# Performance work log

Hardware: AMD Instinct MI355X
Metric: run time of the kernel (lower is better)

Reference implementation:

```python
import jax, jax.numpy as jnp
import numpy as np
from jax import lax

EPS = 1e-5
MIN_SAMPLES = 4
RESHAPE = 14        # edge-map downsample factor
KEEP_FRAC = 0.1     # 1 - quantile(0.9)
KERNEL_FRAC = 0.05  # eval-mode log_kernel

SOBEL_X = jnp.array([[-1., 0., 1.], [-2., 0., 2.], [-1., 0., 1.]], jnp.float32)
SOBEL_Y = jnp.array([[-1., -2., -1.], [0., 0., 0.], [1., 2., 1.]], jnp.float32)


def _dwconv3(x, k):
    C = x.shape[1]
    kern = jnp.broadcast_to(k, (C, 1, 3, 3)).astype(x.dtype)
    return lax.conv_general_dilated(x, kern, (1, 1), 'SAME',
        feature_group_count=C, dimension_numbers=('NCHW', 'OIHW', 'NCHW'))


def _erode3(m):
    k = jnp.ones((1, 1, 3, 3), m.dtype)
    s = lax.conv_general_dilated(m, k, (1, 1), 'SAME',
        dimension_numbers=('NCHW', 'OIHW', 'NCHW'))
    return (s >= 9.0).astype(m.dtype)


def _masked_mean(x, mask, axis=-1):
    m = mask.astype(x.dtype)
    return jnp.sum(x * m, axis=axis) / jnp.maximum(jnp.sum(m, axis=axis), 1.0)


def _ssi_norm(x, mask):
    # scale-shift-invariant normalization: masked median shift, masked MAD scale
    big = jnp.where(mask, x, jnp.inf)
    srt = jnp.sort(big, axis=-1)
    n = jnp.sum(mask, axis=-1)
    idx = jnp.maximum((n - 1) // 2, 0)
    med = jnp.take_along_axis(srt, idx[..., None], axis=-1)
    med = jnp.where(n[..., None] > 0, med, 0.0)
    scale = _masked_mean(jnp.abs(x - med), mask, axis=-1)[..., None]
    return (x - med) / jnp.maximum(scale, EPS)


def _get_edge(image, vmask):
    gx = _dwconv3(image, SOBEL_X) / 8.0
    gy = _dwconv3(image, SOBEL_Y) / 8.0
    gx = jnp.sqrt(jnp.mean(gx * gx, axis=1, keepdims=True))
    gy = jnp.sqrt(jnp.mean(gy * gy, axis=1, keepdims=True))
    edges = jnp.sqrt(gx * gx + gy * gy)
    H, W = edges.shape[-2:]
    bm = jnp.zeros((H, W), edges.dtype).at[3:H - 3, 3:W - 3].set(1.0)
    return edges * bm * vmask


def _resize_bilinear(x, oh, ow):
    # torch F.interpolate bilinear, align_corners=False, no antialias
    B, C, H, W = x.shape
    def coords(o, s):
        c = jnp.clip((jnp.arange(o) + 0.5) * (s / o) - 0.5, 0.0, s - 1.0)
        i0 = jnp.floor(c).astype(jnp.int32)
        return i0, jnp.minimum(i0 + 1, s - 1), c - i0
    y0, y1, wy = coords(oh, H)
    x0, x1, wx = coords(ow, W)
    wy = wy[:, None]; wx = wx[None, :]
    g = lambda yi, xi: x[:, :, yi[:, None], xi[None, :]]
    return (g(y0, x0) * (1 - wy) * (1 - wx) + g(y0, x1) * (1 - wy) * wx
          + g(y1, x0) * wy * (1 - wx) + g(y1, x1) * wy * wx)


def _sample_edges(edges):
    B, _, H, W = edges.shape
    oh, ow = H // RESHAPE, W // RESHAPE
    e = _resize_bilinear(edges, oh, ow).reshape(B, -1)
    k = max(int(KEEP_FRAC * oh * ow), 10)
    _, idx = lax.top_k(e, k)
    return jnp.stack([(idx // ow) * RESHAPE, (idx % ow) * RESHAPE], -1).astype(jnp.int32)


def _extract_patches(x, coords, kh, kw):
    # vectorized irregular patch gather: [B,C,H,W] + [B,P,2] -> [B,P*C,kh*kw]
    B, C, H, W = x.shape
    ph, pw = kh // 2, kw // 2
    xp = jnp.pad(x, ((0, 0), (0, 0), (ph, ph), (pw, pw)))
    dy = jnp.arange(-ph, ph + 1)
    dx = jnp.arange(-pw, pw + 1)
    def one(img, y, x_):
        return img[:, (y + dy)[:, None], (x_ + dx)[None, :]]
    patches = jax.vmap(jax.vmap(one, in_axes=(None, 0, 0)))(
        xp, coords[..., 0] + ph, coords[..., 1] + pw)  # [B,P,C,kh,kw]
    return patches.reshape(B, -1, kh * kw)


def _forward(inp, tgt, mask, image, vmask):
    mask = mask.astype(bool)
    inp = inp.astype(jnp.float32)
    tgt = tgt.astype(jnp.float32)
    B, _, H, W = inp.shape
    vm = _erode3(vmask.astype(jnp.float32))
    edges = _get_edge(image.astype(jnp.float32), vm)
    coords = _sample_edges(edges)
    ks = int(KERNEL_FRAC * min(H, W))
    ks += int(ks % 2 == 0)
    # local patch branch
    pin = _extract_patches(inp, coords, ks, ks)
    ptg = _extract_patches(tgt, coords, ks, ks)
    pmk = _extract_patches(mask.astype(jnp.float32), coords, ks, ks) > 0.5
    pin = _ssi_norm(pin, pmk)
    ptg = _ssi_norm(ptg, pmk)
    err = jnp.maximum(jnp.abs(pin - ptg), EPS)
    valid = jnp.sum(pmk, axis=-1) >= MIN_SAMPLES
    ep = jnp.sqrt(jnp.maximum(_masked_mean(err, pmk, -1), EPS))  # [B,P]
    e_patch = _masked_mean(ep, valid, -1)                         # [B]
    # global image branch
    gi = _ssi_norm(inp.reshape(B, 1, H * W), mask.reshape(B, 1, H * W))
    gt = _ssi_norm(tgt.reshape(B, 1, H * W), mask.reshape(B, 1, H * W))
    gerr = jnp.maximum(jnp.abs(gi - gt), EPS)
    e_glob = jnp.sqrt(jnp.maximum(_masked_mean(gerr, mask.reshape(B, 1, H * W), -1), EPS)).squeeze(-1)
    return 0.5 * (e_patch + e_glob)  # [B]


def setup_inputs() -> dict:
    key = jax.random.key(0)
    k1, k2, k3, k4 = jax.random.split(key, 4)
    B, H, W = 32, 480, 640
    return {
        'input': jax.random.uniform(k1, (B, 1, H, W), jnp.float32, 0.1, 10.0),
        'target': jax.random.uniform(k2, (B, 1, H, W), jnp.float32, 0.1, 10.0),
        'mask': jax.random.bernoulli(k3, 0.9, (B, 1, H, W)),
        'image': jax.random.normal(k4, (B, 3, H, W), jnp.float32),
        'validity_mask': jnp.ones((B, 1, H, W), bool),
    }


def reference(input, target, mask, image, validity_mask):
    return _forward(input, target, mask, image, validity_mask)
```

## Files before the change

kernel.cpp:

```cpp
#include <hip/hip_runtime.h>
#include <math.h>

#define BB 32
#define HH 480
#define WW 640
#define HWN (HH * WW)
#define OH 34
#define OW 45
#define OHW (OH * OW)
#define KTOP 153
#define KS 25
#define PHW 12
#define PATCH (KS * KS)
#define RESHAPE_I 14
#define EPSV 1e-5f

#define TSLICE 10
#define TSW (OHW / TSLICE)

#define NB12 4096
#define PSLICE 32
#define NSLICE 16
#define CAP 32768
#define LCAP 2048
#define CPAD 32

#define EDGE_BLKS ((BB * OHW * 4) / 256)
#define RANK_BLKS (BB * TSLICE)
#define COL_BLKS (BB * 2 * NSLICE)

__device__ __forceinline__ unsigned int fkey(float f) {
  unsigned int u = __float_as_uint(f);
  return (u & 0x80000000u) ? ~u : (u | 0x80000000u);
}
__device__ __forceinline__ float fkey_inv(unsigned int k) {
  unsigned int u = (k & 0x80000000u) ? (k & 0x7FFFFFFFu) : ~k;
  return __uint_as_float(u);
}

__device__ __forceinline__ float breduce256(float v, float* red) {
  const int t = threadIdx.x;
  __syncthreads();
  red[t] = v;
  __syncthreads();
  for (int s2 = 128; s2 > 0; s2 >>= 1) {
    if (t < s2) red[t] += red[t + s2];
    __syncthreads();
  }
  float r = red[0];
  __syncthreads();
  return r;
}

__device__ __forceinline__ float2 breduce256x2(float a, float b, float* red) {
  const int t = threadIdx.x;
  __syncthreads();
  red[t] = a;
  red[256 + t] = b;
  __syncthreads();
  for (int s2 = 128; s2 > 0; s2 >>= 1) {
    if (t < s2) {
      red[t] += red[t + s2];
      red[256 + t] += red[256 + t + s2];
    }
    __syncthreads();
  }
  float2 r = make_float2(red[0], red[256]);
  __syncthreads();
  return r;
}

__device__ float edge_at(const float* __restrict__ image, const unsigned char* __restrict__ vmask,
                         int b, int y, int x) {
  if (y < 3 || y >= HH - 3 || x < 3 || x >= WW - 3) return 0.f;
  const unsigned char* vm = vmask + (size_t)b * HWN;
  #pragma unroll
  for (int dy = -1; dy <= 1; ++dy) {
    #pragma unroll
    for (int dx = -1; dx <= 1; ++dx) {
      if (!vm[(size_t)(y + dy) * WW + (x + dx)]) return 0.f;
    }
  }
  const float* img = image + (size_t)b * 3 * HWN;
  float sx2 = 0.f, sy2 = 0.f;
  #pragma unroll
  for (int c = 0; c < 3; ++c) {
    const float* p = img + (size_t)c * HWN + (size_t)y * WW + x;
    float a00 = p[-WW - 1], a01 = p[-WW], a02 = p[-WW + 1];
    float a10 = p[-1],                    a12 = p[1];
    float a20 = p[WW - 1],  a21 = p[WW],  a22 = p[WW + 1];
    float gx = (-a00 + a02 + -2.f * a10 + 2.f * a12 + -a20 + a22) / 8.f;
    float gy = (-a00 + -2.f * a01 + -a02 + a20 + 2.f * a21 + a22) / 8.f;
    sx2 += gx * gx;
    sy2 += gy * gy;
  }
  float gxm = sqrtf(sx2 / 3.f);
  float gym = sqrtf(sy2 / 3.f);
  return sqrtf(gxm * gxm + gym * gym);
}

__global__ __launch_bounds__(256) void gpass12_kernel(const float* __restrict__ inp,
                                                      const float* __restrict__ tgt,
                                                      const unsigned char* __restrict__ mask,
                                                      unsigned int* __restrict__ ghist) {
  const int b = blockIdx.x / PSLICE;
  const int sl = blockIdx.x % PSLICE;
  const int t = threadIdx.x;
  __shared__ unsigned int hist[2 * NB12];
  for (int i = t; i < 2 * NB12; i += 256) hist[i] = 0;
  __syncthreads();
  const float4* xi4 = (const float4*)(inp + (size_t)b * HWN);
  const float4* xt4 = (const float4*)(tgt + (size_t)b * HWN);
  const unsigned int* m4 = (const unsigned int*)(mask + (size_t)b * HWN);
  const int per4 = (HWN / PSLICE) / 4;
  const int s0 = sl * per4;
  for (int i = s0 + t; i < s0 + per4; i += 256) {
    unsigned int mm = m4[i];
    if (!mm) continue;
    float4 a = xi4[i], c = xt4[i];
    if (mm & 0x000000FFu) { atomicAdd(&hist[fkey(a.x) >> 20], 1u); atomicAdd(&hist[NB12 + (fkey(c.x) >> 20)], 1u); }
    if (mm & 0x0000FF00u) { atomicAdd(&hist[fkey(a.y) >> 20], 1u); atomicAdd(&hist[NB12 + (fkey(c.y) >> 20)], 1u); }
    if (mm & 0x00FF0000u) { atomicAdd(&hist[fkey(a.z) >> 20], 1u); atomicAdd(&hist[NB12 + (fkey(c.z) >> 20)], 1u); }
    if (mm & 0xFF000000u) { atomicAdd(&hist[fkey(a.w) >> 20], 1u); atomicAdd(&hist[NB12 + (fkey(c.w) >> 20)], 1u); }
  }
  __syncthreads();
  for (int i = t; i < NB12; i += 256) {
    unsigned int h0 = hist[i], h1 = hist[NB12 + i];
    if (h0) atomicAdd(&ghist[(size_t)(b * 2 + 0) * NB12 + i], h0);
    if (h1) atomicAdd(&ghist[(size_t)(b * 2 + 1) * NB12 + i], h1);
  }
}

__global__ __launch_bounds__(256) void edge_resize_kernel(const float* __restrict__ image,
                                                          const unsigned char* __restrict__ vmask,
                                                          float* __restrict__ re) {
  int gid = blockIdx.x * 256 + threadIdx.x;
  int corner = gid & 3;
  int cell = gid >> 2;
  int b = cell / OHW;
  int rem = cell % OHW;
  int oy = rem / OW, ox = rem % OW;

  const float ry = (float)((double)HH / (double)OH);
  const float rx = (float)((double)WW / (double)OW);
  float cy = fminf(fmaxf(((float)oy + 0.5f) * ry - 0.5f, 0.f), (float)(HH - 1));
  float cx = fminf(fmaxf(((float)ox + 0.5f) * rx - 0.5f, 0.f), (float)(WW - 1));
  int y0 = (int)floorf(cy);
  int x0 = (int)floorf(cx);
  int y1 = min(y0 + 1, HH - 1);
  int x1 = min(x0 + 1, WW - 1);
  float wy = cy - (float)y0;
  float wx = cx - (float)x0;

  int yy = (corner & 2) ? y1 : y0;
  int xx = (corner & 1) ? x1 : x0;
  float w = ((corner & 2) ? wy : 1.f - wy) * ((corner & 1) ? wx : 1.f - wx);
  float g = edge_at(image, vmask, b, yy, xx) * w;
  g += __shfl_xor(g, 1, 64);
  g += __shfl_xor(g, 2, 64);
  if (corner == 0) re[cell] = g;
}

__global__ __launch_bounds__(256) void k_rank_sel(const float* __restrict__ re,
                                                  const unsigned int* __restrict__ ghist,
                                                  int* __restrict__ rpart,
                                                  int* __restrict__ sel) {
  __shared__ float e[OHW];
  __shared__ unsigned int scan[256];
  const int t = threadIdx.x;
  if (blockIdx.x < RANK_BLKS) {
    const int b = blockIdx.x / TSLICE;
    const int sl = blockIdx.x % TSLICE;
    for (int i = t; i < OHW; i += 256) e[i] = re[b * OHW + i];
    __syncthreads();

    float vi[6];
    int idx[6], cnt[6];
    #pragma unroll
    for (int q = 0; q < 6; ++q) {
      int i = t + q * 256;
      idx[q] = i;
      vi[q] = (i < OHW) ? e[i] : 0.f;
      cnt[q] = 0;
    }
    const int j0 = sl * TSW;
    for (int jj = 0; jj < TSW; ++jj) {
      int j = j0 + jj;
      float u = e[j];
      #pragma unroll
      for (int q = 0; q < 6; ++q) {
        cnt[q] += (u > vi[q]) || (u == vi[q] && j < idx[q]);
      }
    }
    int* rp = rpart + ((size_t)b * TSLICE + sl) * OHW;
    #pragma unroll
    for (int q = 0; q < 6; ++q) {
      if (idx[q] < OHW) rp[idx[q]] = cnt[q];
    }
  } else {
    const int bs = blockIdx.x - RANK_BLKS;
    const unsigned int* gh = ghist + (size_t)bs * NB12;
    unsigned int local[16];
    unsigned int s = 0;
    const int base = t * 16;
    #pragma unroll
    for (int j = 0; j < 16; ++j) {
      local[j] = gh[base + j];
      s += local[j];
    }
    scan[t] = s;
    __syncthreads();
    for (int d = 1; d < 256; d <<= 1) {
      unsigned int v = (t >= d) ? scan[t - d] : 0u;
      __syncthreads();
      scan[t] += v;
      __syncthreads();
    }
    const unsigned int incl = scan[t];
    const unsigned int ex = incl - s;
    const unsigned int n = scan[255];
    if (n == 0) {
      if (t == 0) {
        sel[bs * 4 + 0] = -1;
        sel[bs * 4 + 1] = 0;
        sel[bs * 4 + 2] = 0;
        sel[bs * 4 + 3] = 0;
      }
      return;
    }
    const unsigned int r = (n - 1) >> 1;
    if (r >= ex && r < incl) {
      unsigned int cum = ex;
      int bin = base;
      #pragma unroll
      for (int j = 0; j < 16; ++j) {
        unsigned int h = local[j];
        if (cum + h > r) { bin = base + j; break; }
        cum += h;
      }
      sel[bs * 4 + 0] = bin;
      sel[bs * 4 + 1] = (int)(r - cum);
      sel[bs * 4 + 2] = (int)n;
      sel[bs * 4 + 3] = (int)cum;
    }
  }
}

__global__ __launch_bounds__(256) void k_write_collect(const float* __restrict__ inp,
                                                       const float* __restrict__ tgt,
                                                       const unsigned char* __restrict__ mask,
                                                       const int* __restrict__ sel,
                                                       const int* __restrict__ rpart,
                                                       float* __restrict__ cand,
                                                       unsigned int* __restrict__ ccount,
                                                       float* __restrict__ sbelow,
                                                       float* __restrict__ sabove,
                                                       int* __restrict__ coords) {
  __shared__ float red[512];
  __shared__ float buf[LCAP];
  __shared__ unsigned int lcnt, gbase;
  const int t = threadIdx.x;
  if (blockIdx.x < COL_BLKS) {
    const int bs = blockIdx.x / NSLICE;
    const int sl = blockIdx.x % NSLICE;
    const int b = bs >> 1, s = bs & 1;
    const float* x = (s == 0 ? inp : tgt) + (size_t)b * HWN;
    const unsigned char* m = mask + (size_t)b * HWN;
    const int prefix = sel[bs * 4 + 0];
    if (t == 0) lcnt = 0;
    __syncthreads();
    float sb = 0.f, sa = 0.f;
    if (prefix >= 0) {
      float* cd = cand + (size_t)bs * CAP;
      const float4* x4 = (const float4*)x;
      const unsigned int* m4 = (const unsigned int*)m;
      const int per4 = (HWN / NSLICE) / 4;
      const int s0 = sl * per4;
      for (int i = s0 + t; i < s0 + per4; i += 256) {
        unsigned int mm = m4[i];
        if (!mm) continue;
        float4 a = x4[i];
        #define GCOL(av, bit) \
          if (mm & bit) { \
            float v = av; \
            int pf = (int)(fkey(v) >> 20); \
            if (pf < prefix) sb += v; \
            else if (pf > prefix) sa += v; \
            else { \
              unsigned int pos = atomicAdd(&lcnt, 1u); \
              if (pos < LCAP) buf[pos] = v; \
              else { \
                unsigned int g = atomicAdd(&ccount[bs * CPAD], 1u); \
                if (g < CAP) cd[g] = v; \
              } \
            } \
          }
        GCOL(a.x, 0x000000FFu)
        GCOL(a.y, 0x0000FF00u)
        GCOL(a.z, 0x00FF0000u)
        GCOL(a.w, 0xFF000000u)
        #undef GCOL
      }
    }
    __syncthreads();
    if (prefix >= 0) {
      unsigned int c = min(lcnt, (unsigned int)LCAP);
      if (t == 0 && c > 0) gbase = atomicAdd(&ccount[bs * CPAD], c);
      __syncthreads();
      if (c > 0) {
        float* cd = cand + (size_t)bs * CAP;
        unsigned int base = gbase;
        for (unsigned int i = t; i < c; i += 256) {
          unsigned int pos = base + i;
          if (pos < CAP) cd[pos] = buf[i];
        }
      }
    }
    float2 ts = breduce256x2(sb, sa, red);
    if (t == 0) {
      atomicAdd(&sbelow[bs], ts.x);
      atomicAdd(&sabove[bs], ts.y);
    }
  } else {
    const int b = blockIdx.x - COL_BLKS;
    const int* rp = rpart + (size_t)b * TSLICE * OHW;
    for (int i = t; i < OHW; i += 256) {
      int rank = 0;
      #pragma unroll
      for (int sl = 0; sl < TSLICE; ++sl) rank += rp[sl * OHW + i];
      if (rank < KTOP) {
        coords[(b * KTOP + rank) * 2 + 0] = (i / OW) * RESHAPE_I;
        coords[(b * KTOP + rank) * 2 + 1] = (i % OW) * RESHAPE_I;
      }
    }
  }
}

__global__ __launch_bounds__(64, 4) void patch_kernel(const float* __restrict__ inp,
                                                      const float* __restrict__ tgt,
                                                      const unsigned char* __restrict__ mask,
                                                      const int* __restrict__ coords,
                                                      float* __restrict__ ep, float* __restrict__ val) {
  const int bk = blockIdx.x;
  const int b = bk / KTOP;
  const int t = threadIdx.x;
  __shared__ unsigned int hist[512];
  __shared__ unsigned int sh_pref[2];
  __shared__ int sh_rank[2];

  const int cy = coords[bk * 2 + 0];
  const int cx = coords[bk * 2 + 1];

  float v_in[10], v_tg[10];
  unsigned int mbits = 0;
  #pragma unroll
  for (int q = 0; q < 10; ++q) {
    int i = t + q * 64;
    float vi = 0.f, vt = 0.f;
    if (i < PATCH) {
      int dy = i / KS - PHW, dx = i % KS - PHW;
      int y = cy + dy, x = cx + dx;
      if (y >= 0 && y < HH && x >= 0 && x < WW) {
        size_t off = (size_t)b * HWN + (size_t)y * WW + x;
        if (mask[off]) mbits |= (1u << q);
        vi = inp[off];
        vt = tgt[off];
      }
    }
    v_in[q] = vi; v_tg[q] = vt;
  }

  int pn = __popc(mbits);
  #pragma unroll
  for (int d = 32; d > 0; d >>= 1) pn += __shfl_xor(pn, d, 64);
  const int n = pn;
  const float nf = (float)n;
  const int r = (n > 0) ? ((n - 1) >> 1) : 0;

  if (t == 0) {
    sh_pref[0] = 0; sh_pref[1] = 0;
    sh_rank[0] = r; sh_rank[1] = r;
  }
  __syncthreads();

  #pragma unroll
  for (int p = 0; p < 4; ++p) {
    const int shift = 24 - 8 * p;
    #pragma unroll
    for (int j = 0; j < 8; ++j) hist[t + 64 * j] = 0;
    __syncthreads();
    const int r_in = sh_rank[0], r_tg = sh_rank[1];
    const unsigned int pref_in = sh_pref[0], pref_tg = sh_pref[1];
    #pragma unroll
    for (int q = 0; q < 10; ++q) {
      if (mbits & (1u << q)) {
        unsigned int k = fkey(v_in[q]);
        if (p == 0 || (k >> (shift + 8)) == pref_in)
          atomicAdd(&hist[(k >> shift) & 255u], 1u);
        unsigned int k2 = fkey(v_tg[q]);
        if (p == 0 || (k2 >> (shift + 8)) == pref_tg)
          atomicAdd(&hist[256 + ((k2 >> shift) & 255u)], 1u);
      }
    }
    __syncthreads();
    {
      unsigned int a0 = hist[t * 4 + 0], a1 = hist[t * 4 + 1];
      unsigned int a2 = hist[t * 4 + 2], a3 = hist[t * 4 + 3];
      unsigned int b0 = hist[256 + t * 4 + 0], b1 = hist[256 + t * 4 + 1];
      unsigned int b2 = hist[256 + t * 4 + 2], b3 = hist[256 + t * 4 + 3];
      unsigned int sa0 = a0, sa1 = sa0 + a1, sa2 = sa1 + a2, sa3 = sa2 + a3;
      unsigned int sb0 = b0, sb1 = sb0 + b1, sb2 = sb1 + b2, sb3 = sb2 + b3;
      unsigned int ta = sa3, tb = sb3;
      #pragma unroll
      for (int d = 1; d < 64; d <<= 1) {
        unsigned int ua = (unsigned int)__shfl_up((int)ta, d, 64);
        unsigned int ub = (unsigned int)__shfl_up((int)tb, d, 64);
        if (t >= d) { ta += ua; tb += ub; }
      }
      unsigned int exa = ta - sa3, exb = tb - sb3;
      unsigned int rra = (unsigned int)r_in, rrb = (unsigned int)r_tg;
      unsigned int pa[4] = {exa, exa + sa0, exa + sa1, exa + sa2};
      unsigned int ca[4] = {exa + sa0, exa + sa1, exa + sa2, exa + sa3};
      unsigned int pb[4] = {exb, exb + sb0, exb + sb1, exb + sb2};
      unsigned int cb[4] = {exb + sb0, exb + sb1, exb + sb2, exb + sb3};
      #pragma unroll
      for (int j = 0; j < 4; ++j) {
        if (rra >= pa[j] && rra < ca[j]) {
          sh_pref[0] = (pref_in << 8) | (unsigned int)(t * 4 + j);
          sh_rank[0] = (int)(rra - pa[j]);
        }
        if (rrb >= pb[j] && rrb < cb[j]) {
          sh_pref[1] = (pref_tg << 8) | (unsigned int)(t * 4 + j);
          sh_rank[1] = (int)(rrb - pb[j]);
        }
      }
    }
    __syncthreads();
  }

  const float med_i = (n > 0) ? fkey_inv(sh_pref[0]) : 0.f;
  const float med_t = (n > 0) ? fkey_inv(sh_pref[1]) : 0.f;

  float pi = 0.f, pt = 0.f;
  #pragma unroll
  for (int q = 0; q < 10; ++q) {
    if (mbits & (1u << q)) {
      pi += fabsf(v_in[q] - med_i);
      pt += fabsf(v_tg[q] - med_t);
    }
  }
  #pragma unroll
  for (int d = 32; d > 0; d >>= 1) {
    pi += __shfl_xor(pi, d, 64);
    pt += __shfl_xor(pt, d, 64);
  }
  const float si = fmaxf(pi / fmaxf(nf, 1.f), EPSV);
  const float st = fmaxf(pt / fmaxf(nf, 1.f), EPSV);

  float pe = 0.f;
  #pragma unroll
  for (int q = 0; q < 10; ++q) {
    if (mbits & (1u << q)) {
      float a = (v_in[q] - med_i) / si;
      float c = (v_tg[q] - med_t) / st;
      pe += fmaxf(fabsf(a - c), EPSV);
    }
  }
  #pragma unroll
  for (int d = 32; d > 0; d >>= 1) pe += __shfl_xor(pe, d, 64);

  if (t == 0) {
    ep[bk] = sqrtf(fmaxf(pe / fmaxf(nf, 1.f), EPSV));
    val[bk] = (n >= 4) ? 1.f : 0.f;
  }
}

__global__ __launch_bounds__(256) void k_gfinal_preduce(const float* __restrict__ cand,
                                                        const unsigned int* __restrict__ ccount,
                                                        const int* __restrict__ sel,
                                                        const float* __restrict__ sbelow,
                                                        const float* __restrict__ sabove,
                                                        const float* __restrict__ ep,
                                                        const float* __restrict__ val,
                                                        float* __restrict__ gstats,
                                                        float* __restrict__ nvals,
                                                        float* __restrict__ e_patch) {
  __shared__ unsigned int hist[256];
  __shared__ float red[512];
  __shared__ int sh_bin, sh_r;
  __shared__ float sh_med;
  const int t = threadIdx.x;
  if (blockIdx.x < 64) {
    const int bs = blockIdx.x;
    const int prefix = sel[bs * 4 + 0];
    const int r2 = sel[bs * 4 + 1];
    const int n = sel[bs * 4 + 2];
    const int nbelow = sel[bs * 4 + 3];
    const float* cd = cand + (size_t)bs * CAP;
    int c = (int)min(ccount[bs * CPAD], (unsigned int)CAP);
    if (prefix < 0) {
      if (t == 0) {
        gstats[bs * 2 + 0] = 0.f;
        gstats[bs * 2 + 1] = 0.f;
        if ((bs & 1) == 0) nvals[bs >> 1] = 0.f;
      }
      return;
    }

    hist[t] = 0;
    __syncthreads();
    for (int i = t; i < c; i += 256)
      atomicAdd(&hist[(fkey(cd[i]) >> 12) & 255u], 1u);
    __syncthreads();
    if (t == 0) {
      unsigned int rr = (unsigned int)r2, cum = 0;
      int bin = 0;
      for (; bin < 256; ++bin) {
        unsigned int h = hist[bin];
        if (cum + h > rr) break;
        cum += h;
      }
      sh_bin = bin;
      sh_r = (int)(rr - cum);
    }
    __syncthreads();
    const int bin1 = sh_bin;
    const int r3 = sh_r;

    hist[t] = 0;
    __syncthreads();
    for (int i = t; i < c; i += 256) {
      unsigned int k = fkey(cd[i]);
      if (((k >> 12) & 255u) == (unsigned int)bin1)
        atomicAdd(&hist[(k >> 4) & 255u], 1u);
    }
    __syncthreads();
    if (t == 0) {
      unsigned int rr = (unsigned int)r3, cum = 0;
      int bin = 0;
      for (; bin < 256; ++bin) {
        unsigned int h = hist[bin];
        if (cum + h > rr) break;
        cum += h;
      }
      sh_bin = bin;
      sh_r = (int)(rr - cum);
    }
    __syncthreads();
    const int bin2 = sh_bin;
    const int r4 = sh_r;

    if (t < 16) hist[t] = 0;
    __syncthreads();
    {
      const unsigned int want = (((unsigned int)bin1 << 8) | (unsigned int)bin2);
      for (int i = t; i < c; i += 256) {
        unsigned int k = fkey(cd[i]);
        if (((k >> 4) & 0xFFFFu) == want)
          atomicAdd(&hist[k & 15u], 1u);
      }
    }
    __syncthreads();
    if (t == 0) {
      unsigned int rr = (unsigned int)r4, cum = 0;
      int bin = 0;
      for (; bin < 16; ++bin) {
        unsigned int h = hist[bin];
        if (cum + h > rr) break;
        cum += h;
      }
      unsigned int key = ((unsigned int)prefix << 20) |
                         ((unsigned int)bin1 << 12) |
                         ((unsigned int)bin2 << 4) | (unsigned int)bin;
      sh_med = fkey_inv(key);
    }
    __syncthreads();
    const float med = sh_med;

    float ps = 0.f;
    for (int i = t; i < c; i += 256) ps += fabsf(cd[i] - med);
    float scand = breduce256(ps, red);
    if (t == 0) {
      float nb = (float)nbelow;
      float na = (float)(n - nbelow - c);
      float num = (nb * med - sbelow[bs]) + (sabove[bs] - na * med) + scand;
      gstats[bs * 2 + 0] = med;
      gstats[bs * 2 + 1] = num / fmaxf((float)n, 1.f);
      if ((bs & 1) == 0) nvals[bs >> 1] = (float)n;
    }
  } else {
    const int b = blockIdx.x - 64;
    float se = 0.f, sv = 0.f;
    for (int i = t; i < KTOP; i += 256) {
      float v = val[b * KTOP + i];
      se += ep[b * KTOP + i] * v;
      sv += v;
    }
    float2 tt = breduce256x2(se, sv, red);
    if (t == 0) e_patch[b] = tt.x / fmaxf(tt.y, 1.f);
  }
}

__global__ __launch_bounds__(256) void k_gerr_final(const float* __restrict__ inp,
                                                    const float* __restrict__ tgt,
                                                    const unsigned char* __restrict__ mask,
                                                    const float* __restrict__ gstats,
                                                    const float* __restrict__ nvals,
                                                    const float* __restrict__ e_patch,
                                                    float* __restrict__ gacc,
                                                    unsigned int* __restrict__ gdone,
                                                    float* __restrict__ out) {
  const int b = blockIdx.x / PSLICE;
  const int sl = blockIdx.x % PSLICE;
  __shared__ float red[256];
  const int t = threadIdx.x;
  const float med_i = gstats[(b * 2 + 0) * 2 + 0];
  const float sc_i = fmaxf(gstats[(b * 2 + 0) * 2 + 1], EPSV);
  const float med_t = gstats[(b * 2 + 1) * 2 + 0];
  const float sc_t = fmaxf(gstats[(b * 2 + 1) * 2 + 1], EPSV);
  const float ri = 1.f / sc_i, rt = 1.f / sc_t;
  const float4* xi4 = (const float4*)(inp + (size_t)b * HWN);
  const float4* xt4 = (const float4*)(tgt + (size_t)b * HWN);
  const unsigned int* m4 = (const unsigned int*)(mask + (size_t)b * HWN);
  const int per4 = (HWN / PSLICE) / 4;
  const int s0 = sl * per4;
  float part = 0.f;
  for (int i = s0 + t; i < s0 + per4; i += 256) {
    unsigned int mm = m4[i];
    if (!mm) continue;
    float4 a = xi4[i], c = xt4[i];
    if (mm & 0x000000FFu) part += fmaxf(fabsf((a.x - med_i) * ri - (c.x - med_t) * rt), EPSV);
    if (mm & 0x0000FF00u) part += fmaxf(fabsf((a.y - med_i) * ri - (c.y - med_t) * rt), EPSV);
    if (mm & 0x00FF0000u) part += fmaxf(fabsf((a.z - med_i) * ri - (c.z - med_t) * rt), EPSV);
    if (mm & 0xFF000000u) part += fmaxf(fabsf((a.w - med_i) * ri - (c.w - med_t) * rt), EPSV);
  }
  float tp = breduce256(part, red);
  if (t == 0) {
    atomicAdd(&gacc[b], tp);
    __threadfence();
    unsigned int prev = atomicAdd(&gdone[b], 1u);
    if (prev == PSLICE - 1) {
      __threadfence();
      float g = atomicAdd(&gacc[b], 0.0f);
      float n = nvals[b];
      float eg = sqrtf(fmaxf(g / fmaxf(n, 1.f), EPSV));
      out[b] = 0.5f * (e_patch[b] + eg);
    }
  }
}

extern "C" void kernel_launch(void* const* d_in, const int* in_sizes, int n_in,
                              void* d_out, int out_size, void* d_ws, size_t ws_size,
                              hipStream_t stream) {
  const float* inp = (const float*)d_in[0];
  const float* tgt = (const float*)d_in[1];
  const unsigned char* mask = (const unsigned char*)d_in[2];
  const float* image = (const float*)d_in[3];
  const unsigned char* vmask = (const unsigned char*)d_in[4];
  float* out = (float*)d_out;

  float* ws = (float*)d_ws;
  float* re = ws;
  int* coords = (int*)(ws + 48960);
  float* ep = (float*)(coords + 9792);
  float* val = ep + 4896;
  float* e_patch = val + 4896;
  float* gstats = e_patch + 32;
  float* nvals = gstats + 128;
  int* sel12 = (int*)(nvals + 32);
  int* rpart = sel12 + 256;
  float* cand = (float*)(rpart + 489600);
  unsigned int* ghist12 = (unsigned int*)(cand + (size_t)64 * CAP);
  unsigned int* ccount = ghist12 + (size_t)64 * NB12;
  float* sbelow = (float*)(ccount + 64 * CPAD);
  float* sabove = sbelow + 64;
  float* gacc = sabove + 64;
  unsigned int* gdone = (unsigned int*)(gacc + 32);
  size_t zero_bytes = ((size_t)64 * NB12 + 64 * CPAD + 64 + 64 + 32 + 32) * 4;
  hipMemsetAsync(ghist12, 0, zero_bytes, stream);

  gpass12_kernel<<<BB * PSLICE, 256, 0, stream>>>(inp, tgt, mask, ghist12);
  edge_resize_kernel<<<EDGE_BLKS, 256, 0, stream>>>(image, vmask, re);
  k_rank_sel<<<RANK_BLKS + 64, 256, 0, stream>>>(re, ghist12, rpart, sel12);
  k_write_collect<<<COL_BLKS + BB, 256, 0, stream>>>(inp, tgt, mask, sel12, rpart, cand, ccount,
                                                     sbelow, sabove, coords);
  patch_kernel<<<BB * KTOP, 64, 0, stream>>>(inp, tgt, mask, coords, ep, val);
  k_gfinal_preduce<<<64 + BB, 256, 0, stream>>>(cand, ccount, sel12, sbelow, sabove,
                                                ep, val, gstats, nvals, e_patch);
  k_gerr_final<<<BB * PSLICE, 256, 0, stream>>>(inp, tgt, mask, gstats, nvals, e_patch,
                                                gacc, gdone, out);
}
```

Baseline: 394.2 us.

## Fuse pipeline stages via last-block-done counters to cut kernel launches

Reduces seven kernel launches to four. Dependent reduction steps (median-bin selection, rank summation, median refinement, patch reduction and final combine) now run inside the last block to finish each batch, detected with atomic done-counters and thread fences. The patch and global-error passes are merged into one grid, and the global-error pass uses 64-thread blocks with wave-shuffle reductions. The aim is to remove launch gaps and serialization between small kernels. The cost is tail work done by a single block, plus extra atomics and fences.

New measurement: 610.8 us. +54.9%, slower.

```diff
diff --git a/kernel.cpp b/kernel.cpp
--- a/kernel.cpp
+++ b/kernel.cpp
@@ -21,13 +21,16 @@
 #define NB12 4096
 #define PSLICE 32
 #define NSLICE 16
+#define GS 128
 #define CAP 32768
 #define LCAP 2048
 #define CPAD 32
 
 #define EDGE_BLKS ((BB * OHW * 4) / 256)
+#define COL_BLKS (BB * 2 * NSLICE)
 #define RANK_BLKS (BB * TSLICE)
-#define COL_BLKS (BB * 2 * NSLICE)
+#define PATCH_BLKS (BB * KTOP)
+#define GERR_BLKS (BB * GS)
 
 __device__ __forceinline__ unsigned int fkey(float f) {
   unsigned int u = __float_as_uint(f);
@@ -69,6 +72,8 @@
   __syncthreads();
   return r;
 }
+
+__device__ __forceinline__ float aread(float* p) { return atomicAdd(p, 0.0f); }
 
 __device__ float edge_at(const float* __restrict__ image, const unsigned char* __restrict__ vmask,
                          int b, int y, int x) {
@@ -99,14 +104,17 @@
   return sqrtf(gxm * gxm + gym * gym);
 }
 
-__global__ __launch_bounds__(256) void gpass12_kernel(const float* __restrict__ inp,
-                                                      const float* __restrict__ tgt,
-                                                      const unsigned char* __restrict__ mask,
-                                                      unsigned int* __restrict__ ghist) {
+__global__ __launch_bounds__(256) void k_gpass_sel(const float* __restrict__ inp,
+                                                   const float* __restrict__ tgt,
+                                                   const unsigned char* __restrict__ mask,
+                                                   unsigned int* __restrict__ ghist,
+                                                   unsigned int* __restrict__ hdone,
+                                                   int* __restrict__ sel) {
   const int b = blockIdx.x / PSLICE;
   const int sl = blockIdx.x % PSLICE;
   const int t = threadIdx.x;
   __shared__ unsigned int hist[2 * NB12];
+  __shared__ int sh_last;
   for (int i = t; i < 2 * NB12; i += 256) hist[i] = 0;
   __syncthreads();
   const float4* xi4 = (const float4*)(inp + (size_t)b * HWN);
@@ -129,6 +137,65 @@
     if (h0) atomicAdd(&ghist[(size_t)(b * 2 + 0) * NB12 + i], h0);
     if (h1) atomicAdd(&ghist[(size_t)(b * 2 + 1) * NB12 + i], h1);
   }
+  __syncthreads();
+  if (t == 0) {
+    __threadfence();
+    unsigned int prev = atomicAdd(&hdone[b], 1u);
+    sh_last = (prev == PSLICE - 1) ? 1 : 0;
+  }
+  __syncthreads();
+  if (!sh_last) return;
+  __threadfence();
+
+  unsigned int* scan = hist;
+  for (int s = 0; s < 2; ++s) {
+    const int bs = b * 2 + s;
+    const unsigned int* gh = ghist + (size_t)bs * NB12;
+    unsigned int local[16];
+    unsigned int sm = 0;
+    const int base = t * 16;
+    #pragma unroll
+    for (int j = 0; j < 16; ++j) {
+      local[j] = gh[base + j];
+      sm += local[j];
+    }
+    scan[t] = sm;
+    __syncthreads();
+    for (int d = 1; d < 256; d <<= 1) {
+      unsigned int v = (t >= d) ? scan[t - d] : 0u;
+      __syncthreads();
+      scan[t] += v;
+      __syncthreads();
+    }
+    const unsigned int incl = scan[t];
+    const unsigned int ex = incl - sm;
+    const unsigned int n = scan[255];
+    if (n == 0) {
+      if (t == 0) {
+        sel[bs * 4 + 0] = -1;
+        sel[bs * 4 + 1] = 0;
+        sel[bs * 4 + 2] = 0;
+        sel[bs * 4 + 3] = 0;
+      }
+    } else {
+      const unsigned int r = (n - 1) >> 1;
+      if (r >= ex && r < incl) {
+        unsigned int cum = ex;
+        int bin = base;
+        #pragma unroll
+        for (int j = 0; j < 16; ++j) {
+          unsigned int h = local[j];
+          if (cum + h > r) { bin = base + j; break; }
+          cum += h;
+        }
+        sel[bs * 4 + 0] = bin;
+        sel[bs * 4 + 1] = (int)(r - cum);
+        sel[bs * 4 + 2] = (int)n;
+        sel[bs * 4 + 3] = (int)cum;
+      }
+    }
+    __syncthreads();
+  }
 }
 
 __global__ __launch_bounds__(256) void edge_resize_kernel(const float* __restrict__ image,
@@ -161,105 +228,30 @@
   if (corner == 0) re[cell] = g;
 }
 
-__global__ __launch_bounds__(256) void k_rank_sel(const float* __restrict__ re,
-                                                  const unsigned int* __restrict__ ghist,
-                                                  int* __restrict__ rpart,
-                                                  int* __restrict__ sel) {
-  __shared__ float e[OHW];
-  __shared__ unsigned int scan[256];
-  const int t = threadIdx.x;
-  if (blockIdx.x < RANK_BLKS) {
-    const int b = blockIdx.x / TSLICE;
-    const int sl = blockIdx.x % TSLICE;
-    for (int i = t; i < OHW; i += 256) e[i] = re[b * OHW + i];
-    __syncthreads();
-
-    float vi[6];
-    int idx[6], cnt[6];
-    #pragma unroll
-    for (int q = 0; q < 6; ++q) {
-      int i = t + q * 256;
-      idx[q] = i;
-      vi[q] = (i < OHW) ? e[i] : 0.f;
-      cnt[q] = 0;
-    }
-    const int j0 = sl * TSW;
-    for (int jj = 0; jj < TSW; ++jj) {
-      int j = j0 + jj;
-      float u = e[j];
-      #pragma unroll
-      for (int q = 0; q < 6; ++q) {
-        cnt[q] += (u > vi[q]) || (u == vi[q] && j < idx[q]);
-      }
-    }
-    int* rp = rpart + ((size_t)b * TSLICE + sl) * OHW;
-    #pragma unroll
-    for (int q = 0; q < 6; ++q) {
-      if (idx[q] < OHW) rp[idx[q]] = cnt[q];
-    }
-  } else {
-    const int bs = blockIdx.x - RANK_BLKS;
-    const unsigned int* gh = ghist + (size_t)bs * NB12;
-    unsigned int local[16];
-    unsigned int s = 0;
-    const int base = t * 16;
-    #pragma unroll
-    for (int j = 0; j < 16; ++j) {
-      local[j] = gh[base + j];
-      s += local[j];
-    }
-    scan[t] = s;
-    __syncthreads();
-    for (int d = 1; d < 256; d <<= 1) {
-      unsigned int v = (t >= d) ? scan[t - d] : 0u;
-      __syncthreads();
-      scan[t] += v;
-      __syncthreads();
-    }
-    const unsigned int incl = scan[t];
-    const unsigned int ex = incl - s;
-    const unsigned int n = scan[255];
-    if (n == 0) {
-      if (t == 0) {
-        sel[bs * 4 + 0] = -1;
-        sel[bs * 4 + 1] = 0;
-        sel[bs * 4 + 2] = 0;
-        sel[bs * 4 + 3] = 0;
-      }
-      return;
-    }
-    const unsigned int r = (n - 1) >> 1;
-    if (r >= ex && r < incl) {
-      unsigned int cum = ex;
-      int bin = base;
-      #pragma unroll
-      for (int j = 0; j < 16; ++j) {
-        unsigned int h = local[j];
-        if (cum + h > r) { bin = base + j; break; }
-        cum += h;
-      }
-      sel[bs * 4 + 0] = bin;
-      sel[bs * 4 + 1] = (int)(r - cum);
-      sel[bs * 4 + 2] = (int)n;
-      sel[bs * 4 + 3] = (int)cum;
-    }
-  }
-}
-
-__global__ __launch_bounds__(256) void k_write_collect(const float* __restrict__ inp,
-                                                       const float* __restrict__ tgt,
-                                                       const unsigned char* __restrict__ mask,
-                                                       const int* __restrict__ sel,
-                                                       const int* __restrict__ rpart,
-                                                       float* __restrict__ cand,
-                                                       unsigned int* __restrict__ ccount,
-                                                       float* __restrict__ sbelow,
-                                                       float* __restrict__ sabove,
-                                                       int* __restrict__ coords) {
+__global__ __launch_bounds__(256) void k_rank_collect(const float* __restrict__ inp,
+                                                      const float* __restrict__ tgt,
+                                                      const unsigned char* __restrict__ mask,
+                                                      const int* __restrict__ sel,
+                                                      const float* __restrict__ re,
+                                                      int* __restrict__ rpart,
+                                                      float* __restrict__ cand,
+                                                      unsigned int* __restrict__ ccount,
+                                                      float* __restrict__ sbelow,
+                                                      float* __restrict__ sabove,
+                                                      int* __restrict__ coords,
+                                                      unsigned int* __restrict__ cdone,
+                                                      unsigned int* __restrict__ rdone,
+                                                      float* __restrict__ gstats,
+                                                      float* __restrict__ nvals) {
   __shared__ float red[512];
   __shared__ float buf[LCAP];
+  __shared__ float e[OHW];
+  __shared__ unsigned int ghisto[256];
   __shared__ unsigned int lcnt, gbase;
+  __shared__ int sh_bin, sh_r, sh_last;
+  __shared__ float sh_med;
   const int t = threadIdx.x;
+
   if (blockIdx.x < COL_BLKS) {
     const int bs = blockIdx.x / NSLICE;
     const int sl = blockIdx.x % NSLICE;
@@ -321,13 +313,157 @@
       atomicAdd(&sbelow[bs], ts.x);
       atomicAdd(&sabove[bs], ts.y);
     }
+    __syncthreads();
+    if (t == 0) {
+      __threadfence();
+      unsigned int prev = atomicAdd(&cdone[bs], 1u);
+      sh_last = (prev == NSLICE - 1) ? 1 : 0;
+    }
+    __syncthreads();
+    if (!sh_last) return;
+    __threadfence();
+
+    {
+      const int r2 = sel[bs * 4 + 1];
+      const int n = sel[bs * 4 + 2];
+      const int nbelow = sel[bs * 4 + 3];
+      const float* cd = cand + (size_t)bs * CAP;
+      int c = (int)min(ccount[bs * CPAD], (unsigned int)CAP);
+      if (prefix < 0) {
+        if (t == 0) {
+          gstats[bs * 2 + 0] = 0.f;
+          gstats[bs * 2 + 1] = 0.f;
+          if ((bs & 1) == 0) nvals[bs >> 1] = 0.f;
+        }
+        return;
+      }
+      ghisto[t] = 0;
+      __syncthreads();
+      for (int i = t; i < c; i += 256)
+        atomicAdd(&ghisto[(fkey(cd[i]) >> 12) & 255u], 1u);
+      __syncthreads();
+      if (t == 0) {
+        unsigned int rr = (unsigned int)r2, cum = 0;
+        int bin = 0;
+        for (; bin < 256; ++bin) {
+          unsigned int h = ghisto[bin];
+          if (cum + h > rr) break;
+          cum += h;
+        }
+        sh_bin = bin;
+        sh_r = (int)(rr - cum);
+      }
+      __syncthreads();
+      const int bin1 = sh_bin;
+      const int r3 = sh_r;
+
+      ghisto[t] = 0;
+      __syncthreads();
+      for (int i = t; i < c; i += 256) {
+        unsigned int k = fkey(cd[i]);
+        if (((k >> 12) & 255u) == (unsigned int)bin1)
+          atomicAdd(&ghisto[(k >> 4) & 255u], 1u);
+      }
+      __syncthreads();
+      if (t == 0) {
+        unsigned int rr = (unsigned int)r3, cum = 0;
+        int bin = 0;
+        for (; bin < 256; ++bin) {
+          unsigned int h = ghisto[bin];
+          if (cum + h > rr) break;
+          cum += h;
+        }
+        sh_bin = bin;
+        sh_r = (int)(rr - cum);
+      }
+      __syncthreads();
+      const int bin2 = sh_bin;
+      const int r4 = sh_r;
+
+      if (t < 16) ghisto[t] = 0;
+      __syncthreads();
+      {
+        const unsigned int want = (((unsigned int)bin1 << 8) | (unsigned int)bin2);
+        for (int i = t; i < c; i += 256) {
+          unsigned int k = fkey(cd[i]);
+          if (((k >> 4) & 0xFFFFu) == want)
+            atomicAdd(&ghisto[k & 15u], 1u);
+        }
+      }
+      __syncthreads();
+      if (t == 0) {
+        unsigned int rr = (unsigned int)r4, cum = 0;
+        int bin = 0;
+        for (; bin < 16; ++bin) {
+          unsigned int h = ghisto[bin];
+          if (cum + h > rr) break;
+          cum += h;
+        }
+        unsigned int key = ((unsigned int)prefix << 20) |
+                           ((unsigned int)bin1 << 12) |
+                           ((unsigned int)bin2 << 4) | (unsigned int)bin;
+        sh_med = fkey_inv(key);
+      }
+      __syncthreads();
+      const float med = sh_med;
+
+      float ps = 0.f;
+      for (int i = t; i < c; i += 256) ps += fabsf(cd[i] - med);
+      float scand = breduce256(ps, red);
+      if (t == 0) {
+        float nb = (float)nbelow;
+        float na = (float)(n - nbelow - c);
+        float num = (nb * med - aread(&sbelow[bs])) + (aread(&sabove[bs]) - na * med) + scand;
+        gstats[bs * 2 + 0] = med;
+        gstats[bs * 2 + 1] = num / fmaxf((float)n, 1.f);
+        if ((bs & 1) == 0) nvals[bs >> 1] = (float)n;
+      }
+    }
   } else {
-    const int b = blockIdx.x - COL_BLKS;
-    const int* rp = rpart + (size_t)b * TSLICE * OHW;
+    const int blk = blockIdx.x - COL_BLKS;
+    const int b = blk / TSLICE;
+    const int sl = blk % TSLICE;
+    for (int i = t; i < OHW; i += 256) e[i] = re[b * OHW + i];
+    __syncthreads();
+
+    float vi[6];
+    int idx[6], cnt[6];
+    #pragma unroll
+    for (int q = 0; q < 6; ++q) {
+      int i = t + q * 256;
+      idx[q] = i;
+      vi[q] = (i < OHW) ? e[i] : 0.f;
+      cnt[q] = 0;
+    }
+    const int j0 = sl * TSW;
+    for (int jj = 0; jj < TSW; ++jj) {
+      int j = j0 + jj;
+      float u = e[j];
+      #pragma unroll
+      for (int q = 0; q < 6; ++q) {
+        cnt[q] += (u > vi[q]) || (u == vi[q] && j < idx[q]);
+      }
+    }
+    int* rp = rpart + ((size_t)b * TSLICE + sl) * OHW;
+    #pragma unroll
+    for (int q = 0; q < 6; ++q) {
+      if (idx[q] < OHW) rp[idx[q]] = cnt[q];
+    }
+    __syncthreads();
+    if (t == 0) {
+      __threadfence();
+      unsigned int prev = atomicAdd(&rdone[b], 1u);
+      sh_last = (prev == TSLICE - 1) ? 1 : 0;
+    }
+    __syncthreads();
+    if (!sh_last) return;
+    __threadfence();
+
+    const int* rp2 = rpart + (size_t)b * TSLICE * OHW;
     for (int i = t; i < OHW; i += 256) {
       int rank = 0;
       #pragma unroll
-      for (int sl = 0; sl < TSLICE; ++sl) rank += rp[sl * OHW + i];
+      for (int sl2 = 0; sl2 < TSLICE; ++sl2) rank += rp2[sl2 * OHW + i];
       if (rank < KTOP) {
         coords[(b * KTOP + rank) * 2 + 0] = (i / OW) * RESHAPE_I;
         coords[(b * KTOP + rank) * 2 + 1] = (i % OW) * RESHAPE_I;
@@ -336,315 +472,202 @@
   }
 }
 
-__global__ __launch_bounds__(64, 4) void patch_kernel(const float* __restrict__ inp,
+__device__ __forceinline__ void finalize_b(int b, float* __restrict__ gacc,
+                                           float* __restrict__ epnum, float* __restrict__ epden,
+                                           const float* __restrict__ nvals,
+                                           float* __restrict__ out) {
+  __threadfence();
+  float g = aread(&gacc[b]);
+  float en = aread(&epnum[b]);
+  float ed = aread(&epden[b]);
+  float n = nvals[b];
+  float epb = en / fmaxf(ed, 1.f);
+  float eg = sqrtf(fmaxf(g / fmaxf(n, 1.f), EPSV));
+  out[b] = 0.5f * (epb + eg);
+}
+
+__global__ __launch_bounds__(64, 4) void k_patch_gerr(const float* __restrict__ inp,
                                                       const float* __restrict__ tgt,
                                                       const unsigned char* __restrict__ mask,
                                                       const int* __restrict__ coords,
-                                                      float* __restrict__ ep, float* __restrict__ val) {
-  const int bk = blockIdx.x;
-  const int b = bk / KTOP;
+                                                      const float* __restrict__ gstats,
+                                                      const float* __restrict__ nvals,
+                                                      float* __restrict__ epnum,
+                                                      float* __restrict__ epden,
+                                                      float* __restrict__ gacc,
+                                                      unsigned int* __restrict__ gdone,
+                                                      float* __restrict__ out) {
   const int t = threadIdx.x;
-  __shared__ unsigned int hist[512];
-  __shared__ unsigned int sh_pref[2];
-  __shared__ int sh_rank[2];
-
-  const int cy = coords[bk * 2 + 0];
-  const int cx = coords[bk * 2 + 1];
-
-  float v_in[10], v_tg[10];
-  unsigned int mbits = 0;
-  #pragma unroll
-  for (int q = 0; q < 10; ++q) {
-    int i = t + q * 64;
-    float vi = 0.f, vt = 0.f;
-    if (i < PATCH) {
-      int dy = i / KS - PHW, dx = i % KS - PHW;
-      int y = cy + dy, x = cx + dx;
-      if (y >= 0 && y < HH && x >= 0 && x < WW) {
-        size_t off = (size_t)b * HWN + (size_t)y * WW + x;
-        if (mask[off]) mbits |= (1u << q);
-        vi = inp[off];
-        vt = tgt[off];
-      }
-    }
-    v_in[q] = vi; v_tg[q] = vt;
-  }
-
-  int pn = __popc(mbits);
-  #pragma unroll
-  for (int d = 32; d > 0; d >>= 1) pn += __shfl_xor(pn, d, 64);
-  const int n = pn;
-  const float nf = (float)n;
-  const int r = (n > 0) ? ((n - 1) >> 1) : 0;
-
-  if (t == 0) {
-    sh_pref[0] = 0; sh_pref[1] = 0;
-    sh_rank[0] = r; sh_rank[1] = r;
-  }
-  __syncthreads();
-
-  #pragma unroll
-  for (int p = 0; p < 4; ++p) {
-    const int shift = 24 - 8 * p;
-    #pragma unroll
-    for (int j = 0; j < 8; ++j) hist[t + 64 * j] = 0;
-    __syncthreads();
-    const int r_in = sh_rank[0], r_tg = sh_rank[1];
-    const unsigned int pref_in = sh_pref[0], pref_tg = sh_pref[1];
+  if (blockIdx.x < PATCH_BLKS) {
+    const int bk = blockIdx.x;
+    const int b = bk / KTOP;
+    __shared__ unsigned int hist[512];
+    __shared__ unsigned int sh_pref[2];
+    __shared__ int sh_rank[2];
+
+    const int cy = coords[bk * 2 + 0];
+    const int cx = coords[bk * 2 + 1];
+
+    float v_in[10], v_tg[10];
+    unsigned int mbits = 0;
+    #pragma unroll
+    for (int q = 0; q < 10; ++q) {
+      int i = t + q * 64;
+      float vi = 0.f, vt = 0.f;
+      if (i < PATCH) {
+        int dy = i / KS - PHW, dx = i % KS - PHW;
+        int y = cy + dy, x = cx + dx;
+        if (y >= 0 && y < HH && x >= 0 && x < WW) {
+          size_t off = (size_t)b * HWN + (size_t)y * WW + x;
+          if (mask[off]) mbits |= (1u << q);
+          vi = inp[off];
+          vt = tgt[off];
+        }
+      }
+      v_in[q] = vi; v_tg[q] = vt;
+    }
+
+    int pn = __popc(mbits);
+    #pragma unroll
+    for (int d = 32; d > 0; d >>= 1) pn += __shfl_xor(pn, d, 64);
+    const int n = pn;
+    const float nf = (float)n;
+    const int r = (n > 0) ? ((n - 1) >> 1) : 0;
+
+    if (t == 0) {
+      sh_pref[0] = 0; sh_pref[1] = 0;
+      sh_rank[0] = r; sh_rank[1] = r;
+    }
+    __syncthreads();
+
+    #pragma unroll
+    for (int p = 0; p < 4; ++p) {
+      const int shift = 24 - 8 * p;
+      #pragma unroll
+      for (int j = 0; j < 8; ++j) hist[t + 64 * j] = 0;
+      __syncthreads();
+      const int r_in = sh_rank[0], r_tg = sh_rank[1];
+      const unsigned int pref_in = sh_pref[0], pref_tg = sh_pref[1];
+      #pragma unroll
+      for (int q = 0; q < 10; ++q) {
+        if (mbits & (1u << q)) {
+          unsigned int k = fkey(v_in[q]);
+          if (p == 0 || (k >> (shift + 8)) == pref_in)
+            atomicAdd(&hist[(k >> shift) & 255u], 1u);
+          unsigned int k2 = fkey(v_tg[q]);
+          if (p == 0 || (k2 >> (shift + 8)) == pref_tg)
+            atomicAdd(&hist[256 + ((k2 >> shift) & 255u)], 1u);
+        }
+      }
+      __syncthreads();
+      {
+        unsigned int a0 = hist[t * 4 + 0], a1 = hist[t * 4 + 1];
+        unsigned int a2 = hist[t * 4 + 2], a3 = hist[t * 4 + 3];
+        unsigned int b0 = hist[256 + t * 4 + 0], b1 = hist[256 + t * 4 + 1];
+        unsigned int b2 = hist[256 + t * 4 + 2], b3 = hist[256 + t * 4 + 3];
+        unsigned int sa0 = a0, sa1 = sa0 + a1, sa2 = sa1 + a2, sa3 = sa2 + a3;
+        unsigned int sb0 = b0, sb1 = sb0 + b1, sb2 = sb1 + b2, sb3 = sb2 + b3;
+        unsigned int ta = sa3, tb = sb3;
+        #pragma unroll
+        for (int d = 1; d < 64; d <<= 1) {
+          unsigned int ua = (unsigned int)__shfl_up((int)ta, d, 64);
+          unsigned int ub = (unsigned int)__shfl_up((int)tb, d, 64);
+          if (t >= d) { ta += ua; tb += ub; }
+        }
+        unsigned int exa = ta - sa3, exb = tb - sb3;
+        unsigned int rra = (unsigned int)r_in, rrb = (unsigned int)r_tg;
+        unsigned int pa[4] = {exa, exa + sa0, exa + sa1, exa + sa2};
+        unsigned int ca[4] = {exa + sa0, exa + sa1, exa + sa2, exa + sa3};
+        unsigned int pb[4] = {exb, exb + sb0, exb + sb1, exb + sb2};
+        unsigned int cb[4] = {exb + sb0, exb + sb1, exb + sb2, exb + sb3};
+        #pragma unroll
+        for (int j = 0; j < 4; ++j) {
+          if (rra >= pa[j] && rra < ca[j]) {
+            sh_pref[0] = (pref_in << 8) | (unsigned int)(t * 4 + j);
+            sh_rank[0] = (int)(rra - pa[j]);
+          }
+          if (rrb >= pb[j] && rrb < cb[j]) {
+            sh_pref[1] = (pref_tg << 8) | (unsigned int)(t * 4 + j);
+            sh_rank[1] = (int)(rrb - pb[j]);
+          }
+        }
+      }
+      __syncthreads();
+    }
+
+    const float med_i = (n > 0) ? fkey_inv(sh_pref[0]) : 0.f;
+    const float med_t = (n > 0) ? fkey_inv(sh_pref[1]) : 0.f;
+
+    float pi = 0.f, pt = 0.f;
     #pragma unroll
     for (int q = 0; q < 10; ++q) {
       if (mbits & (1u << q)) {
-        unsigned int k = fkey(v_in[q]);
-        if (p == 0 || (k >> (shift + 8)) == pref_in)
-          atomicAdd(&hist[(k >> shift) & 255u], 1u);
-        unsigned int k2 = fkey(v_tg[q]);
-        if (p == 0 || (k2 >> (shift + 8)) == pref_tg)
-          atomicAdd(&hist[256 + ((k2 >> shift) & 255u)], 1u);
-      }
-    }
-    __syncthreads();
-    {
-      unsigned int a0 = hist[t * 4 + 0], a1 = hist[t * 4 + 1];
-      unsigned int a2 = hist[t * 4 + 2], a3 = hist[t * 4 + 3];
-      unsigned int b0 = hist[256 + t * 4 + 0], b1 = hist[256 + t * 4 + 1];
-      unsigned int b2 = hist[256 + t * 4 + 2], b3 = hist[256 + t * 4 + 3];
-      unsigned int sa0 = a0, sa1 = sa0 + a1, sa2 = sa1 + a2, sa3 = sa2 + a3;
-      unsigned int sb0 = b0, sb1 = sb0 + b1, sb2 = sb1 + b2, sb3 = sb2 + b3;
-      unsigned int ta = sa3, tb = sb3;
-      #pragma unroll
-      for (int d = 1; d < 64; d <<= 1) {
-        unsigned int ua = (unsigned int)__shfl_up((int)ta, d, 64);
-        unsigned int ub = (unsigned int)__shfl_up((int)tb, d, 64);
-        if (t >= d) { ta += ua; tb += ub; }
-      }
-      unsigned int exa = ta - sa3, exb = tb - sb3;
-      unsigned int rra = (unsigned int)r_in, rrb = (unsigned int)r_tg;
-      unsigned int pa[4] = {exa, exa + sa0, exa + sa1, exa + sa2};
-      unsigned int ca[4] = {exa + sa0, exa + sa1, exa + sa2, exa + sa3};
-      unsigned int pb[4] = {exb, exb + sb0, exb + sb1, exb + sb2};
-      unsigned int cb[4] = {exb + sb0, exb + sb1, exb + sb2, exb + sb3};
-      #pragma unroll
-      for (int j = 0; j < 4; ++j) {
-        if (rra >= pa[j] && rra < ca[j]) {
-          sh_pref[0] = (pref_in << 8) | (unsigned int)(t * 4 + j);
-          sh_rank[0] = (int)(rra - pa[j]);
-        }
-        if (rrb >= pb[j] && rrb < cb[j]) {
-          sh_pref[1] = (pref_tg << 8) | (unsigned int)(t * 4 + j);
-          sh_rank[1] = (int)(rrb - pb[j]);
-        }
-      }
-    }
-    __syncthreads();
-  }
-
-  const float med_i = (n > 0) ? fkey_inv(sh_pref[0]) : 0.f;
-  const float med_t = (n > 0) ? fkey_inv(sh_pref[1]) : 0.f;
-
-  float pi = 0.f, pt = 0.f;
-  #pragma unroll
-  for (int q = 0; q < 10; ++q) {
-    if (mbits & (1u << q)) {
-      pi += fabsf(v_in[q] - med_i);
-      pt += fabsf(v_tg[q] - med_t);
-    }
-  }
-  #pragma unroll
-  for (int d = 32; d > 0; d >>= 1) {
-    pi += __shfl_xor(pi, d, 64);
-    pt += __shfl_xor(pt, d, 64);
-  }
-  const float si = fmaxf(pi / fmaxf(nf, 1.f), EPSV);
-  const float st = fmaxf(pt / fmaxf(nf, 1.f), EPSV);
-
-  float pe = 0.f;
-  #pragma unroll
-  for (int q = 0; q < 10; ++q) {
-    if (mbits & (1u << q)) {
-      float a = (v_in[q] - med_i) / si;
-      float c = (v_tg[q] - med_t) / st;
-      pe += fmaxf(fabsf(a - c), EPSV);
-    }
-  }
-  #pragma unroll
-  for (int d = 32; d > 0; d >>= 1) pe += __shfl_xor(pe, d, 64);
-
-  if (t == 0) {
-    ep[bk] = sqrtf(fmaxf(pe / fmaxf(nf, 1.f), EPSV));
-    val[bk] = (n >= 4) ? 1.f : 0.f;
-  }
-}
-
-__global__ __launch_bounds__(256) void k_gfinal_preduce(const float* __restrict__ cand,
-                                                        const unsigned int* __restrict__ ccount,
-                                                        const int* __restrict__ sel,
-                                                        const float* __restrict__ sbelow,
-                                                        const float* __restrict__ sabove,
-                                                        const float* __restrict__ ep,
-                                                        const float* __restrict__ val,
-                                                        float* __restrict__ gstats,
-                                                        float* __restrict__ nvals,
-                                                        float* __restrict__ e_patch) {
-  __shared__ unsigned int hist[256];
-  __shared__ float red[512];
-  __shared__ int sh_bin, sh_r;
-  __shared__ float sh_med;
-  const int t = threadIdx.x;
-  if (blockIdx.x < 64) {
-    const int bs = blockIdx.x;
-    const int prefix = sel[bs * 4 + 0];
-    const int r2 = sel[bs * 4 + 1];
-    const int n = sel[bs * 4 + 2];
-    const int nbelow = sel[bs * 4 + 3];
-    const float* cd = cand + (size_t)bs * CAP;
-    int c = (int)min(ccount[bs * CPAD], (unsigned int)CAP);
-    if (prefix < 0) {
-      if (t == 0) {
-        gstats[bs * 2 + 0] = 0.f;
-        gstats[bs * 2 + 1] = 0.f;
-        if ((bs & 1) == 0) nvals[bs >> 1] = 0.f;
-      }
-      return;
-    }
-
-    hist[t] = 0;
-    __syncthreads();
-    for (int i = t; i < c; i += 256)
-      atomicAdd(&hist[(fkey(cd[i]) >> 12) & 255u], 1u);
-    __syncthreads();
+        pi += fabsf(v_in[q] - med_i);
+        pt += fabsf(v_tg[q] - med_t);
+      }
+    }
+    #pragma unroll
+    for (int d = 32; d > 0; d >>= 1) {
+      pi += __shfl_xor(pi, d, 64);
+      pt += __shfl_xor(pt, d, 64);
+    }
+    const float si = fmaxf(pi / fmaxf(nf, 1.f), EPSV);
+    const float st = fmaxf(pt / fmaxf(nf, 1.f), EPSV);
+
+    float pe = 0.f;
+    #pragma unroll
+    for (int q = 0; q < 10; ++q) {
+      if (mbits & (1u << q)) {
+        float a = (v_in[q] - med_i) / si;
+        float c = (v_tg[q] - med_t) / st;
+        pe += fmaxf(fabsf(a - c), EPSV);
+      }
+    }
+    #pragma unroll
+    for (int d = 32; d > 0; d >>= 1) pe += __shfl_xor(pe, d, 64);
+
     if (t == 0) {
-      unsigned int rr = (unsigned int)r2, cum = 0;
-      int bin = 0;
-      for (; bin < 256; ++bin) {
-        unsigned int h = hist[bin];
-        if (cum + h > rr) break;
-        cum += h;
-      }
-      sh_bin = bin;
-      sh_r = (int)(rr - cum);
-    }
-    __syncthreads();
-    const int bin1 = sh_bin;
-    const int r3 = sh_r;
-
-    hist[t] = 0;
-    __syncthreads();
-    for (int i = t; i < c; i += 256) {
-      unsigned int k = fkey(cd[i]);
-      if (((k >> 12) & 255u) == (unsigned int)bin1)
-        atomicAdd(&hist[(k >> 4) & 255u], 1u);
-    }
-    __syncthreads();
+      float valf = (n >= 4) ? 1.f : 0.f;
+      float epv = sqrtf(fmaxf(pe / fmaxf(nf, 1.f), EPSV));
+      atomicAdd(&epnum[b], epv * valf);
+      atomicAdd(&epden[b], valf);
+      __threadfence();
+      unsigned int prev = atomicAdd(&gdone[b], 1u);
+      if (prev == (unsigned int)(KTOP + GS - 1))
+        finalize_b(b, gacc, epnum, epden, nvals, out);
+    }
+  } else {
+    const int task = blockIdx.x - PATCH_BLKS;
+    const int b = task / GS;
+    const int sl = task % GS;
+    const float med_i = gstats[(b * 2 + 0) * 2 + 0];
+    const float sc_i = fmaxf(gstats[(b * 2 + 0) * 2 + 1], EPSV);
+    const float med_t = gstats[(b * 2 + 1) * 2 + 0];
+    const float sc_t = fmaxf(gstats[(b * 2 + 1) * 2 + 1], EPSV);
+    const float ri = 1.f / sc_i, rt = 1.f / sc_t;
+    const float4* xi4 = (const float4*)(inp + (size_t)b * HWN);
+    const float4* xt4 = (const float4*)(tgt + (size_t)b * HWN);
+    const unsigned int* m4 = (const unsigned int*)(mask + (size_t)b * HWN);
+    const int per4 = (HWN / GS) / 4;
+    const int s0 = sl * per4;
+    float part = 0.f;
+    for (int i = s0 + t; i < s0 + per4; i += 64) {
+      unsigned int mm = m4[i];
+      if (!mm) continue;
+      float4 a = xi4[i], c = xt4[i];
+      if (mm & 0x000000FFu) part += fmaxf(fabsf((a.x - med_i) * ri - (c.x - med_t) * rt), EPSV);
+      if (mm & 0x0000FF00u) part += fmaxf(fabsf((a.y - med_i) * ri - (c.y - med_t) * rt), EPSV);
+      if (mm & 0x00FF0000u) part += fmaxf(fabsf((a.z - med_i) * ri - (c.z - med_t) * rt), EPSV);
+      if (mm & 0xFF000000u) part += fmaxf(fabsf((a.w - med_i) * ri - (c.w - med_t) * rt), EPSV);
+    }
+    #pragma unroll
+    for (int d = 32; d > 0; d >>= 1) part += __shfl_xor(part, d, 64);
     if (t == 0) {
-      unsigned int rr = (unsigned int)r3, cum = 0;
-      int bin = 0;
-      for (; bin < 256; ++bin) {
-        unsigned int h = hist[bin];
-        if (cum + h > rr) break;
-        cum += h;
-      }
-      sh_bin = bin;
-      sh_r = (int)(rr - cum);
-    }
-    __syncthreads();
-    const int bin2 = sh_bin;
-    const int r4 = sh_r;
-
-    if (t < 16) hist[t] = 0;
-    __syncthreads();
-    {
-      const unsigned int want = (((unsigned int)bin1 << 8) | (unsigned int)bin2);
-      for (int i = t; i < c; i += 256) {
-        unsigned int k = fkey(cd[i]);
-        if (((k >> 4) & 0xFFFFu) == want)
-          atomicAdd(&hist[k & 15u], 1u);
-      }
-    }
-    __syncthreads();
-    if (t == 0) {
-      unsigned int rr = (unsigned int)r4, cum = 0;
-      int bin = 0;
-      for (; bin < 16; ++bin) {
-        unsigned int h = hist[bin];
-        if (cum + h > rr) break;
-        cum += h;
-      }
-      unsigned int key = ((unsigned int)prefix << 20) |
-                         ((unsigned int)bin1 << 12) |
-                         ((unsigned int)bin2 << 4) | (unsigned int)bin;
-      sh_med = fkey_inv(key);
-    }
-    __syncthreads();
-    const float med = sh_med;
-
-    float ps = 0.f;
-    for (int i = t; i < c; i += 256) ps += fabsf(cd[i] - med);
-    float scand = breduce256(ps, red);
-    if (t == 0) {
-      float nb = (float)nbelow;
-      float na = (float)(n - nbelow - c);
-      float num = (nb * med - sbelow[bs]) + (sabove[bs] - na * med) + scand;
-      gstats[bs * 2 + 0] = med;
-      gstats[bs * 2 + 1] = num / fmaxf((float)n, 1.f);
-      if ((bs & 1) == 0) nvals[bs >> 1] = (float)n;
-    }
-  } else {
-    const int b = blockIdx.x - 64;
-    float se = 0.f, sv = 0.f;
-    for (int i = t; i < KTOP; i += 256) {
-      float v = val[b * KTOP + i];
-      se += ep[b * KTOP + i] * v;
-      sv += v;
-    }
-    float2 tt = breduce256x2(se, sv, red);
-    if (t == 0) e_patch[b] = tt.x / fmaxf(tt.y, 1.f);
-  }
-}
-
-__global__ __launch_bounds__(256) void k_gerr_final(const float* __restrict__ inp,
-                                                    const float* __restrict__ tgt,
-                                                    const unsigned char* __restrict__ mask,
-                                                    const float* __restrict__ gstats,
-                                                    const float* __restrict__ nvals,
-                                                    const float* __restrict__ e_patch,
-                                                    float* __restrict__ gacc,
-                                                    unsigned int* __restrict__ gdone,
-                                                    float* __restrict__ out) {
-  const int b = blockIdx.x / PSLICE;
-  const int sl = blockIdx.x % PSLICE;
-  __shared__ float red[256];
-  const int t = threadIdx.x;
-  const float med_i = gstats[(b * 2 + 0) * 2 + 0];
-  const float sc_i = fmaxf(gstats[(b * 2 + 0) * 2 + 1], EPSV);
-  const float med_t = gstats[(b * 2 + 1) * 2 + 0];
-  const float sc_t = fmaxf(gstats[(b * 2 + 1) * 2 + 1], EPSV);
-  const float ri = 1.f / sc_i, rt = 1.f / sc_t;
-  const float4* xi4 = (const float4*)(inp + (size_t)b * HWN);
-  const float4* xt4 = (const float4*)(tgt + (size_t)b * HWN);
-  const unsigned int* m4 = (const unsigned int*)(mask + (size_t)b * HWN);
-  const int per4 = (HWN / PSLICE) / 4;
-  const int s0 = sl * per4;
-  float part = 0.f;
-  for (int i = s0 + t; i < s0 + per4; i += 256) {
-    unsigned int mm = m4[i];
-    if (!mm) continue;
-    float4 a = xi4[i], c = xt4[i];
-    if (mm & 0x000000FFu) part += fmaxf(fabsf((a.x - med_i) * ri - (c.x - med_t) * rt), EPSV);
-    if (mm & 0x0000FF00u) part += fmaxf(fabsf((a.y - med_i) * ri - (c.y - med_t) * rt), EPSV);
-    if (mm & 0x00FF0000u) part += fmaxf(fabsf((a.z - med_i) * ri - (c.z - med_t) * rt), EPSV);
-    if (mm & 0xFF000000u) part += fmaxf(fabsf((a.w - med_i) * ri - (c.w - med_t) * rt), EPSV);
-  }
-  float tp = breduce256(part, red);
-  if (t == 0) {
-    atomicAdd(&gacc[b], tp);
-    __threadfence();
-    unsigned int prev = atomicAdd(&gdone[b], 1u);
-    if (prev == PSLICE - 1) {
+      atomicAdd(&gacc[b], part);
       __threadfence();
-      float g = atomicAdd(&gacc[b], 0.0f);
-      float n = nvals[b];
-      float eg = sqrtf(fmaxf(g / fmaxf(n, 1.f), EPSV));
-      out[b] = 0.5f * (e_patch[b] + eg);
+      unsigned int prev = atomicAdd(&gdone[b], 1u);
+      if (prev == (unsigned int)(KTOP + GS - 1))
+        finalize_b(b, gacc, epnum, epden, nvals, out);
     }
   }
 }
@@ -662,10 +685,7 @@
   float* ws = (float*)d_ws;
   float* re = ws;
   int* coords = (int*)(ws + 48960);
-  float* ep = (float*)(coords + 9792);
-  float* val = ep + 4896;
-  float* e_patch = val + 4896;
-  float* gstats = e_patch + 32;
+  float* gstats = (float*)(coords + 9792);
   float* nvals = gstats + 128;
   int* sel12 = (int*)(nvals + 32);
   int* rpart = sel12 + 256;
@@ -676,17 +696,20 @@
   float* sabove = sbelow + 64;
   float* gacc = sabove + 64;
   unsigned int* gdone = (unsigned int*)(gacc + 32);
-  size_t zero_bytes = ((size_t)64 * NB12 + 64 * CPAD + 64 + 64 + 32 + 32) * 4;
+  float* epnum = (float*)(gdone + 32);
+  float* epden = epnum + 32;
+  unsigned int* hdone = (unsigned int*)(epden + 32);
+  unsigned int* rdone = hdone + 32;
+  unsigned int* cdone = rdone + 32;
+  size_t zero_bytes = ((size_t)64 * NB12 + 64 * CPAD + 64 + 64 +
+                       32 + 32 + 32 + 32 + 32 + 32 + 64) * 4;
   hipMemsetAsync(ghist12, 0, zero_bytes, stream);
 
-  gpass12_kernel<<<BB * PSLICE, 256, 0, stream>>>(inp, tgt, mask, ghist12);
+  k_gpass_sel<<<BB * PSLICE, 256, 0, stream>>>(inp, tgt, mask, ghist12, hdone, sel12);
   edge_resize_kernel<<<EDGE_BLKS, 256, 0, stream>>>(image, vmask, re);
-  k_rank_sel<<<RANK_BLKS + 64, 256, 0, stream>>>(re, ghist12, rpart, sel12);
-  k_write_collect<<<COL_BLKS + BB, 256, 0, stream>>>(inp, tgt, mask, sel12, rpart, cand, ccount,
-                                                     sbelow, sabove, coords);
-  patch_kernel<<<BB * KTOP, 64, 0, stream>>>(inp, tgt, mask, coords, ep, val);
-  k_gfinal_preduce<<<64 + BB, 256, 0, stream>>>(cand, ccount, sel12, sbelow, sabove,
-                                                ep, val, gstats, nvals, e_patch);
-  k_gerr_final<<<BB * PSLICE, 256, 0, stream>>>(inp, tgt, mask, gstats, nvals, e_patch,
-                                                gacc, gdone, out);
-}
+  k_rank_collect<<<COL_BLKS + RANK_BLKS, 256, 0, stream>>>(inp, tgt, mask, sel12, re, rpart,
+                                                           cand, ccount, sbelow, sabove, coords,
+                                                           cdone, rdone, gstats, nvals);
+  k_patch_gerr<<<PATCH_BLKS + GERR_BLKS, 64, 0, stream>>>(inp, tgt, mask, coords, gstats, nvals,
+                                                          epnum, epden, gacc, gdone, out);
+}
```
